# Kernel tuning notes

Hardware: AMD Instinct MI355X
Metric: run time of the kernel (lower is better)

The kernel has to match this reference:

```python
import jax, jax.numpy as jnp
import numpy as np

B, L, D_IN = 32, 200, 64
H = 64          # hidden_size
A = 36          # attention_size
NEG_SLOPE = 0.01  # torch LeakyReLU default


def setup_inputs() -> dict:
    key = jax.random.key(0)
    ks = jax.random.split(key, 7)
    s_ln = 1.0 / np.sqrt(D_IN)
    s_w1 = 1.0 / np.sqrt(3 * H)
    s_w2 = 1.0 / np.sqrt(A)
    return {
        "x": jax.random.normal(ks[0], (B, L, D_IN), dtype=jnp.float32),
        "ln_w": jax.random.uniform(ks[1], (D_IN, H), minval=-s_ln, maxval=s_ln, dtype=jnp.float32),
        "ln_b": jax.random.uniform(ks[2], (H,), minval=-s_ln, maxval=s_ln, dtype=jnp.float32),
        "w1": jax.random.uniform(ks[3], (3 * H, A), minval=-s_w1, maxval=s_w1, dtype=jnp.float32),
        "b1": jax.random.uniform(ks[4], (A,), minval=-s_w1, maxval=s_w1, dtype=jnp.float32),
        "w2": jax.random.uniform(ks[5], (A,), minval=-s_w2, maxval=s_w2, dtype=jnp.float32),
        "b2": jax.random.uniform(ks[6], (), minval=-s_w2, maxval=s_w2, dtype=jnp.float32),
    }


def reference(x, ln_w, ln_b, w1, b1, w2, b2):
    # x: [B, L, D_in] -> h: [B, L, H]
    h = jnp.einsum("bld,dh->blh", x, ln_w) + ln_b
    Ld = h.shape[1]
    Hd = h.shape[-1]
    # The torch code concatenates (x1, x2, x1*x2) where x1[b,i,j]=h[b,j],
    # x2[b,i,j]=h[b,i]. Split w1 accordingly instead of materializing the
    # [B,L,L,3H] concat tensor.
    w1a, w1b, w1c = w1[:Hd], w1[Hd:2 * Hd], w1[2 * Hd:]
    a = jnp.einsum("bjh,ha->bja", h, w1a)          # x1 contribution (depends on j)
    c = jnp.einsum("bih,ha->bia", h, w1b)          # x2 contribution (depends on i)
    cross = jnp.einsum("bih,bjh,ha->bija", h, h, w1c)  # (x1*x2) contribution
    pre = a[:, None, :, :] + c[:, :, None, :] + cross + b1   # [B,L,L,A]
    act = jax.nn.leaky_relu(pre, negative_slope=NEG_SLOPE)
    score = jnp.einsum("bija,a->bij", act, w2) + b2          # [B,L,L]
    mask = jnp.tril(jnp.ones((Ld, Ld), dtype=score.dtype))   # causal (incl. diag)
    score = score * mask
    return jnp.einsum("bij,bjh->bih", score, h)               # [B,L,H]
```

## Files before the change

kernel.cpp:

```cpp
#include <hip/hip_runtime.h>

#define B 32
#define L 200
#define DIN 64
#define H 64
#define A 36

typedef __attribute__((ext_vector_type(8))) short short8;
typedef __attribute__((ext_vector_type(4))) float floatx4;
typedef __attribute__((ext_vector_type(8))) float floatx8;

static __device__ __forceinline__ short f2bf(float f) {
    union { float f; unsigned u; } v; v.f = f;
    unsigned r = (v.u + 0x7FFF + ((v.u >> 16) & 1)) >> 16;
    return (short)r;
}

__global__ __launch_bounds__(256) void prep_kernel(
    const float* __restrict__ x, const float* __restrict__ ln_w,
    const float* __restrict__ ln_b, const float* __restrict__ w1,
    float* __restrict__ h_out, float* __restrict__ cc_out, short* __restrict__ hb16_out,
    float* __restrict__ w1a_r, float* __restrict__ w1c_r)
{
    int wave = threadIdx.x >> 6;
    int lane = threadIdx.x & 63;
    int bl = __builtin_amdgcn_readfirstlane(blockIdx.x * 4 + wave);
    const float* xr = x + (size_t)bl * DIN;
    float p0 = ln_b[lane], p1 = 0.f;
    #pragma unroll
    for (int d = 0; d < DIN; d += 2) {
        p0 = fmaf(xr[d],     ln_w[d * H + lane],       p0);
        p1 = fmaf(xr[d + 1], ln_w[(d + 1) * H + lane], p1);
    }
    float acc = p0 + p1;
    __shared__ float hrow[4][H];
    hrow[wave][lane] = acc;
    h_out[(size_t)bl * H + lane] = acc;
    int j = bl % L;
    hb16_out[(size_t)bl * H + (lane ^ ((j & 7) << 3))] = f2bf(acc);
    if (lane < A) {
        float s0 = 0.f, s1 = 0.f;
        #pragma unroll
        for (int hh = 0; hh < H; hh += 2) {
            s0 = fmaf(hrow[wave][hh],     w1[(H + hh) * A + lane],     s0);
            s1 = fmaf(hrow[wave][hh + 1], w1[(H + hh + 1) * A + lane], s1);
        }
        cc_out[(size_t)bl * A + lane] = s0 + s1;
    }
    if (blockIdx.x == 0) {
        for (int idx = threadIdx.x; idx < 2 * 3 * 64 * 8; idx += 256) {
            int e = idx & 7, ln = (idx >> 3) & 63, sn = idx >> 9;
            int s = sn / 3, n = sn - 3 * s;
            int k = s * 32 + (ln >> 4) * 8 + e;
            int c = n * 16 + (ln & 15);
            w1a_r[idx] = (c < A) ? w1[k * A + c] : 0.f;
            w1c_r[idx] = (c < A) ? w1[(2 * H + k) * A + c] : 0.f;
        }
    }
}

__global__ __launch_bounds__(256) void score_kernel(
    const float* __restrict__ h, const short* __restrict__ hb16,
    const float* __restrict__ cc, const float* __restrict__ w1a_r,
    const float* __restrict__ w1c_r, const float* __restrict__ b1,
    const float* __restrict__ w2, const float* __restrict__ b2,
    float* __restrict__ out)
{
    int blk = blockIdx.x;
    int b  = blk / 50;
    int bg = 49 - (blk - b * 50);
    int wave = threadIdx.x >> 6;
    int lane = threadIdx.x & 63;
    int i = __builtin_amdgcn_readfirstlane(bg + 50 * wave);
    int l15 = lane & 15, l4 = lane >> 4;

    __shared__ __align__(16) short tile[208 * 64];

    const short* hb16b = hb16 + (size_t)b * L * H;
    const float* h_b   = h + (size_t)b * L * H;

    int maxrow = bg + 150;
    int nch = (((maxrow | 15) + 1) + 7) >> 3;
    for (int c = wave; c < 8; c += 4) {
        int j = c * 8 + (lane >> 3);
        const short* src = hb16b + (size_t)j * H + (lane & 7) * 8;
        __builtin_amdgcn_global_load_lds(
            (const __attribute__((address_space(1))) void*)src,
            (__attribute__((address_space(3))) void*)&tile[c * 512],
            16, 0, 0);
    }

    const float* hi = h_b + (size_t)i * H;
    float b2v = b2[0];
    float ccl = (lane < A) ? (cc[((size_t)b * L + i) * A + lane] + b1[lane]) : 0.f;
    float w2l = (lane < A) ? w2[lane] : 0.f;
    float w2v[3][4], cbv[3][4];
    #pragma unroll
    for (int n = 0; n < 3; ++n) {
        #pragma unroll
        for (int r = 0; r < 4; ++r) {
            int a = n * 16 + l4 * 4 + r;
            cbv[n][r] = __shfl(ccl, a, 64);
            w2v[n][r] = __shfl(w2l, a, 64);
        }
    }
    short8 afrag[2][3];
    #pragma unroll
    for (int s = 0; s < 2; ++s) {
        float hik[8];
        #pragma unroll
        for (int e = 0; e < 8; ++e) hik[e] = hi[s * 32 + l4 * 8 + e];
        #pragma unroll
        for (int n = 0; n < 3; ++n) {
            floatx8 wa = *(const floatx8*)&w1a_r[(((s * 3 + n) * 64) + lane) * 8];
            floatx8 wc = *(const floatx8*)&w1c_r[(((s * 3 + n) * 64) + lane) * 8];
            #pragma unroll
            for (int e = 0; e < 8; ++e)
                afrag[s][n][e] = f2bf(fmaf(hik[e], wc[e], wa[e]));
        }
    }
    __syncthreads();

    for (int c = 8 + wave; c < nch; c += 4) {
        int j = c * 8 + (lane >> 3); if (j > L - 1) j = L - 1;
        const short* src = hb16b + (size_t)j * H + (lane & 7) * 8;
        __builtin_amdgcn_global_load_lds(
            (const __attribute__((address_space(1))) void*)src,
            (__attribute__((address_space(3))) void*)&tile[c * 512],
            16, 0, 0);
    }

    float oacc[4] = {0.f, 0.f, 0.f, 0.f};
    int mmax = (i >> 4) + 1;
    int mlim1 = mmax < 4 ? mmax : 4;

    #pragma unroll 1
    for (int phase = 0; phase < 2; ++phase) {
        int m0   = phase ? 4 : 0;
        int mend = phase ? mmax : mlim1;
        for (int m = m0; m < mend; ++m) {
            int row = m * 16 + l15;
            const short* brow = tile + row * 64;
            int sw = (l15 & 7) << 3;
            short8 bf0 = *(const short8*)(brow + ((l4 * 8) ^ sw));
            short8 bf1 = *(const short8*)(brow + ((32 + l4 * 8) ^ sw));
            floatx4 c0 = {cbv[0][0], cbv[0][1], cbv[0][2], cbv[0][3]};
            floatx4 c1 = {cbv[1][0], cbv[1][1], cbv[1][2], cbv[1][3]};
            floatx4 c2 = {cbv[2][0], cbv[2][1], cbv[2][2], cbv[2][3]};
            c0 = __builtin_amdgcn_mfma_f32_16x16x32_bf16(afrag[0][0], bf0, c0, 0, 0, 0);
            c1 = __builtin_amdgcn_mfma_f32_16x16x32_bf16(afrag[0][1], bf0, c1, 0, 0, 0);
            c2 = __builtin_amdgcn_mfma_f32_16x16x32_bf16(afrag[0][2], bf0, c2, 0, 0, 0);
            c0 = __builtin_amdgcn_mfma_f32_16x16x32_bf16(afrag[1][0], bf1, c0, 0, 0, 0);
            c1 = __builtin_amdgcn_mfma_f32_16x16x32_bf16(afrag[1][1], bf1, c1, 0, 0, 0);
            c2 = __builtin_amdgcn_mfma_f32_16x16x32_bf16(afrag[1][2], bf1, c2, 0, 0, 0);
            float sp0 = 0.f, sp1 = 0.f, sp2 = 0.f;
            #pragma unroll
            for (int r = 0; r < 4; ++r) {
                sp0 = fmaf(fmaxf(c0[r], 0.01f * c0[r]), w2v[0][r], sp0);
                sp1 = fmaf(fmaxf(c1[r], 0.01f * c1[r]), w2v[1][r], sp1);
                sp2 = fmaf(fmaxf(c2[r], 0.01f * c2[r]), w2v[2][r], sp2);
            }
            float sp = (sp0 + sp1) + sp2;
            sp += __shfl_xor(sp, 16, 64);
            sp += __shfl_xor(sp, 32, 64);
            float sc = (row <= i) ? sp + b2v : 0.f;

            const float* hjb = h_b + (size_t)(m * 16) * H + lane;
            #pragma unroll
            for (int rb = 0; rb < 4; ++rb) {
                #pragma unroll
                for (int q = 0; q < 4; ++q) {
                    int jq = rb * 4 + q;
                    float sq = __int_as_float(
                        __builtin_amdgcn_readlane(__float_as_int(sc), jq));
                    float hv = hjb[jq * H];
                    oacc[rb] = fmaf(sq, hv, oacc[rb]);
                }
            }
        }
        if (phase == 0) __syncthreads();
    }

    out[((size_t)b * L + i) * H + lane] = (oacc[0] + oacc[1]) + (oacc[2] + oacc[3]);
}

extern "C" void kernel_launch(void* const* d_in, const int* in_sizes, int n_in,
                              void* d_out, int out_size, void* d_ws, size_t ws_size,
                              hipStream_t stream) {
    const float* x    = (const float*)d_in[0];
    const float* ln_w = (const float*)d_in[1];
    const float* ln_b = (const float*)d_in[2];
    const float* w1   = (const float*)d_in[3];
    const float* b1   = (const float*)d_in[4];
    const float* w2   = (const float*)d_in[5];
    const float* b2   = (const float*)d_in[6];
    float* out = (float*)d_out;

    float* h_ws   = (float*)d_ws;
    float* cc_ws  = h_ws + (size_t)B * L * H;
    short* hb16_ws = (short*)(cc_ws + (size_t)B * L * A);
    float* w1a_r  = (float*)(hb16_ws + (size_t)B * L * H);
    float* w1c_r  = w1a_r + 3072;

    prep_kernel<<<(B * L) / 4, 256, 0, stream>>>(x, ln_w, ln_b, w1, h_ws, cc_ws,
                                                 hb16_ws, w1a_r, w1c_r);
    score_kernel<<<B * 50, 256, 0, stream>>>(h_ws, hb16_ws, cc_ws, w1a_r, w1c_r,
                                             b1, w2, b2, out);
}
```

Before: 45.32 us.

## Assign contiguous rows per block and software-prefetch B fragments from LDS

Each block now handles four consecutive query rows (4g..4g+3) instead of rows spaced 50 apart. It therefore loads only the prefix of the bf16 h tile it needs in a single pass and drops the two-phase load/sync scheme. The inner loop double-buffers the LDS B-fragment reads for the next 16-row tile so they overlap with the MFMA work. The trade-off is more imbalanced work per block: each block's cost grows with g instead of being roughly equalised across blocks. The whole tile load now also sits before the first barrier rather than overlapping the first iterations.

After: 38.28 us. 1.18x faster.

```diff
diff --git a/kernel.cpp b/kernel.cpp
--- a/kernel.cpp
+++ b/kernel.cpp
@@ -68,10 +68,10 @@
 {
     int blk = blockIdx.x;
     int b  = blk / 50;
-    int bg = 49 - (blk - b * 50);
+    int g  = 49 - (blk - b * 50);
     int wave = threadIdx.x >> 6;
     int lane = threadIdx.x & 63;
-    int i = __builtin_amdgcn_readfirstlane(bg + 50 * wave);
+    int i = __builtin_amdgcn_readfirstlane(4 * g + wave);
     int l15 = lane & 15, l4 = lane >> 4;
 
     __shared__ __align__(16) short tile[208 * 64];
@@ -79,10 +79,10 @@
     const short* hb16b = hb16 + (size_t)b * L * H;
     const float* h_b   = h + (size_t)b * L * H;
 
-    int maxrow = bg + 150;
+    int maxrow = 4 * g + 3;
     int nch = (((maxrow | 15) + 1) + 7) >> 3;
-    for (int c = wave; c < 8; c += 4) {
-        int j = c * 8 + (lane >> 3);
+    for (int c = wave; c < nch; c += 4) {
+        int j = c * 8 + (lane >> 3); if (j > L - 1) j = L - 1;
         const short* src = hb16b + (size_t)j * H + (lane & 7) * 8;
         __builtin_amdgcn_global_load_lds(
             (const __attribute__((address_space(1))) void*)src,
@@ -121,64 +121,57 @@
     }
     __syncthreads();
 
-    for (int c = 8 + wave; c < nch; c += 4) {
-        int j = c * 8 + (lane >> 3); if (j > L - 1) j = L - 1;
-        const short* src = hb16b + (size_t)j * H + (lane & 7) * 8;
-        __builtin_amdgcn_global_load_lds(
-            (const __attribute__((address_space(1))) void*)src,
-            (__attribute__((address_space(3))) void*)&tile[c * 512],
-            16, 0, 0);
-    }
-
     float oacc[4] = {0.f, 0.f, 0.f, 0.f};
     int mmax = (i >> 4) + 1;
-    int mlim1 = mmax < 4 ? mmax : 4;
-
-    #pragma unroll 1
-    for (int phase = 0; phase < 2; ++phase) {
-        int m0   = phase ? 4 : 0;
-        int mend = phase ? mmax : mlim1;
-        for (int m = m0; m < mend; ++m) {
-            int row = m * 16 + l15;
-            const short* brow = tile + row * 64;
-            int sw = (l15 & 7) << 3;
-            short8 bf0 = *(const short8*)(brow + ((l4 * 8) ^ sw));
-            short8 bf1 = *(const short8*)(brow + ((32 + l4 * 8) ^ sw));
-            floatx4 c0 = {cbv[0][0], cbv[0][1], cbv[0][2], cbv[0][3]};
-            floatx4 c1 = {cbv[1][0], cbv[1][1], cbv[1][2], cbv[1][3]};
-            floatx4 c2 = {cbv[2][0], cbv[2][1], cbv[2][2], cbv[2][3]};
-            c0 = __builtin_amdgcn_mfma_f32_16x16x32_bf16(afrag[0][0], bf0, c0, 0, 0, 0);
-            c1 = __builtin_amdgcn_mfma_f32_16x16x32_bf16(afrag[0][1], bf0, c1, 0, 0, 0);
-            c2 = __builtin_amdgcn_mfma_f32_16x16x32_bf16(afrag[0][2], bf0, c2, 0, 0, 0);
-            c0 = __builtin_amdgcn_mfma_f32_16x16x32_bf16(afrag[1][0], bf1, c0, 0, 0, 0);
-            c1 = __builtin_amdgcn_mfma_f32_16x16x32_bf16(afrag[1][1], bf1, c1, 0, 0, 0);
-            c2 = __builtin_amdgcn_mfma_f32_16x16x32_bf16(afrag[1][2], bf1, c2, 0, 0, 0);
-            float sp0 = 0.f, sp1 = 0.f, sp2 = 0.f;
+    int sw = (l15 & 7) << 3;
+
+    const short* brow0 = tile + l15 * 64;
+    short8 bfc0 = *(const short8*)(brow0 + ((l4 * 8) ^ sw));
+    short8 bfc1 = *(const short8*)(brow0 + ((32 + l4 * 8) ^ sw));
+
+    for (int m = 0; m < mmax; ++m) {
+        short8 bfn0, bfn1;
+        if (m + 1 < mmax) {
+            const short* brown = tile + ((m + 1) * 16 + l15) * 64;
+            bfn0 = *(const short8*)(brown + ((l4 * 8) ^ sw));
+            bfn1 = *(const short8*)(brown + ((32 + l4 * 8) ^ sw));
+        }
+        int row = m * 16 + l15;
+        floatx4 c0 = {cbv[0][0], cbv[0][1], cbv[0][2], cbv[0][3]};
+        floatx4 c1 = {cbv[1][0], cbv[1][1], cbv[1][2], cbv[1][3]};
+        floatx4 c2 = {cbv[2][0], cbv[2][1], cbv[2][2], cbv[2][3]};
+        c0 = __builtin_amdgcn_mfma_f32_16x16x32_bf16(afrag[0][0], bfc0, c0, 0, 0, 0);
+        c1 = __builtin_amdgcn_mfma_f32_16x16x32_bf16(afrag[0][1], bfc0, c1, 0, 0, 0);
+        c2 = __builtin_amdgcn_mfma_f32_16x16x32_bf16(afrag[0][2], bfc0, c2, 0, 0, 0);
+        c0 = __builtin_amdgcn_mfma_f32_16x16x32_bf16(afrag[1][0], bfc1, c0, 0, 0, 0);
+        c1 = __builtin_amdgcn_mfma_f32_16x16x32_bf16(afrag[1][1], bfc1, c1, 0, 0, 0);
+        c2 = __builtin_amdgcn_mfma_f32_16x16x32_bf16(afrag[1][2], bfc1, c2, 0, 0, 0);
+        float sp0 = 0.f, sp1 = 0.f, sp2 = 0.f;
+        #pragma unroll
+        for (int r = 0; r < 4; ++r) {
+            sp0 = fmaf(fmaxf(c0[r], 0.01f * c0[r]), w2v[0][r], sp0);
+            sp1 = fmaf(fmaxf(c1[r], 0.01f * c1[r]), w2v[1][r], sp1);
+            sp2 = fmaf(fmaxf(c2[r], 0.01f * c2[r]), w2v[2][r], sp2);
+        }
+        float sp = (sp0 + sp1) + sp2;
+        sp += __shfl_xor(sp, 16, 64);
+        sp += __shfl_xor(sp, 32, 64);
+        float sc = (row <= i) ? sp + b2v : 0.f;
+
+        const float* hjb = h_b + (size_t)(m * 16) * H + lane;
+        #pragma unroll
+        for (int rb = 0; rb < 4; ++rb) {
             #pragma unroll
-            for (int r = 0; r < 4; ++r) {
-                sp0 = fmaf(fmaxf(c0[r], 0.01f * c0[r]), w2v[0][r], sp0);
-                sp1 = fmaf(fmaxf(c1[r], 0.01f * c1[r]), w2v[1][r], sp1);
-                sp2 = fmaf(fmaxf(c2[r], 0.01f * c2[r]), w2v[2][r], sp2);
+            for (int q = 0; q < 4; ++q) {
+                int jq = rb * 4 + q;
+                float sq = __int_as_float(
+                    __builtin_amdgcn_readlane(__float_as_int(sc), jq));
+                float hv = hjb[jq * H];
+                oacc[rb] = fmaf(sq, hv, oacc[rb]);
             }
-            float sp = (sp0 + sp1) + sp2;
-            sp += __shfl_xor(sp, 16, 64);
-            sp += __shfl_xor(sp, 32, 64);
-            float sc = (row <= i) ? sp + b2v : 0.f;
-
-            const float* hjb = h_b + (size_t)(m * 16) * H + lane;
-            #pragma unroll
-            for (int rb = 0; rb < 4; ++rb) {
-                #pragma unroll
-                for (int q = 0; q < 4; ++q) {
-                    int jq = rb * 4 + q;
-                    float sq = __int_as_float(
-                        __builtin_amdgcn_readlane(__float_as_int(sc), jq));
-                    float hv = hjb[jq * H];
-                    oacc[rb] = fmaf(sq, hv, oacc[rb]);
-                }
-            }
-        }
-        if (phase == 0) __syncthreads();
+        }
+        bfc0 = bfn0;
+        bfc1 = bfn1;
     }
 
     out[((size_t)b * L + i) * H + lane] = (oacc[0] + oacc[1]) + (oacc[2] + oacc[3]);
```
